# Performance work log

Measured on AMD Instinct MI355X. Metric: run time of the kernel, lower is better.

Reference implementation:

```python
import jax, jax.numpy as jnp
import numpy as np

DIM = 1024
NUM_HEADS = 16
HEAD_DIM = DIM // NUM_HEADS
SCALE = HEAD_DIM ** -0.5
HIDDEN = int(DIM * 1.0)


def setup_inputs() -> dict:
    key = jax.random.key(0)
    ks = jax.random.split(key, 11)
    s = 0.02
    return {
        "x":  jax.random.normal(ks[0], (2, 2048, DIM), jnp.float32),
        "Wq": jax.random.normal(ks[1], (DIM, DIM), jnp.float32) * s,
        "bq": jnp.zeros((DIM,), jnp.float32),
        "Wk": jax.random.normal(ks[2], (DIM, DIM), jnp.float32) * s,
        "bk": jnp.zeros((DIM,), jnp.float32),
        "Wv": jax.random.normal(ks[3], (DIM, DIM), jnp.float32) * s,
        "bv": jnp.zeros((DIM,), jnp.float32),
        "W1": jax.random.normal(ks[4], (HIDDEN, DIM), jnp.float32) * s,
        "b1": jnp.zeros((HIDDEN,), jnp.float32),
        "W2": jax.random.normal(ks[5], (DIM, HIDDEN), jnp.float32) * s,
        "b2": jnp.zeros((DIM,), jnp.float32),
    }


def _split_heads(t, B, S):
    # [B,S,C] -> [B,H,S,hd]
    return t.reshape(B, S, NUM_HEADS, HEAD_DIM).transpose(0, 2, 1, 3)


def reference(x, Wq, bq, Wk, bk, Wv, bv, W1, b1, W2, b2):
    B, S, C = x.shape
    q = _split_heads(x @ Wq.T + bq, B, S) * SCALE
    k = _split_heads(x @ Wk.T + bk, B, S)
    v = _split_heads(x @ Wv.T + bv, B, S)
    # softmax-free bilinear attention, scores in float32 (matches .float())
    attn = jnp.einsum('bhqd,bhkd->bhqk', q.astype(jnp.float32), k.astype(jnp.float32))
    out = jnp.einsum('bhqk,bhkd->bhqd', attn, v)  # [B,H,S,hd]
    out = out.transpose(0, 2, 1, 3).reshape(B, S, C)
    h = jax.nn.gelu(out @ W1.T + b1, approximate=False)
    mlp = h @ W2.T + b2
    return x + out + mlp
```

## Files before the change

### kernel.cpp

```cpp
#include <hip/hip_runtime.h>
#include <math.h>

#define DIM    1024
#define BATCH  2
#define SEQ    2048
#define NHEAD  16
#define HDIM   64
#define MROWS  (BATCH*SEQ)
#define NSPLIT 8

typedef unsigned short u16;
typedef __attribute__((ext_vector_type(8))) short  s16x8;
typedef __attribute__((ext_vector_type(4))) float  f32x4;

__device__ __forceinline__ float bf2f(u16 h) {
    unsigned u = ((unsigned)h) << 16; float f; __builtin_memcpy(&f, &u, 4); return f;
}
__device__ __forceinline__ u16 f2bf(float f) {
    unsigned u; __builtin_memcpy(&u, &f, 4);
    u += 0x7FFFu + ((u >> 16) & 1u);
    return (u16)(u >> 16);
}

__device__ __forceinline__ void glds16(const u16* g, u16* l) {
    __builtin_amdgcn_global_load_lds(
        (const __attribute__((address_space(1))) void*)g,
        (__attribute__((address_space(3))) void*)l, 16, 0, 0);
}

__global__ __launch_bounds__(256)
void pack_all(const float* __restrict__ x,
              const float* __restrict__ Wq, const float* __restrict__ Wk,
              const float* __restrict__ Wv, const float* __restrict__ W1,
              const float* __restrict__ W2,
              u16* __restrict__ xb, u16* __restrict__ Wqb, u16* __restrict__ Wkb,
              u16* __restrict__ Wvb, u16* __restrict__ W1b, u16* __restrict__ W2b)
{
    const int bid = blockIdx.x;
    const float* src; u16* dst; int i;
    if (bid < 4096) { src = x; dst = xb; i = bid * 256 + threadIdx.x; }
    else {
        const int w = (bid - 4096) >> 10;
        const int lb = (bid - 4096) & 1023;
        src = (w == 0) ? Wq : (w == 1) ? Wk : (w == 2) ? Wv : (w == 3) ? W1 : W2;
        dst = (w == 0) ? Wqb : (w == 1) ? Wkb : (w == 2) ? Wvb : (w == 3) ? W1b : W2b;
        i = lb * 256 + threadIdx.x;
    }
    float4 v = ((const float4*)src)[i];
    ushort4 o = { f2bf(v.x), f2bf(v.y), f2bf(v.z), f2bf(v.w) };
    ((ushort4*)dst)[i] = o;
}

__device__ __forceinline__ void gemm_core_pf128(const u16* __restrict__ Ab,
                                                const u16* __restrict__ Bb,
                                                u16* As, u16* Bs,
                                                int tid, f32x4 acc[4][4])
{
    const int w = tid >> 6, l = tid & 63;
    const int wm = (w >> 1) * 64, wn = (w & 1) * 64;
    const int lr = l & 15, kq = l >> 4;

    const int srow = w * 16 + (l >> 2);
    const int scol = (l & 3) * 8;
    const u16* gA = Ab + (size_t)srow * DIM + scol;
    const u16* gB = Bb + (size_t)srow * DIM + scol;
    const int sdst = w * 512;

    glds16(gA,      As + sdst);         glds16(gA + 64 * DIM,      As + 2048 + sdst);
    glds16(gB,      Bs + sdst);         glds16(gB + 64 * DIM,      Bs + 2048 + sdst);
    glds16(gA + 32, As + 4096 + sdst);  glds16(gA + 32 + 64 * DIM, As + 4096 + 2048 + sdst);
    glds16(gB + 32, Bs + 4096 + sdst);  glds16(gB + 32 + 64 * DIM, Bs + 4096 + 2048 + sdst);

    const int NIT = DIM / 32;
    int cur = 0, nxt2 = 2;
    for (int it = 0; it < NIT; ++it) {
        if (it < NIT - 1) { asm volatile("s_waitcnt vmcnt(4)" ::: "memory"); }
        else              { asm volatile("s_waitcnt vmcnt(0)" ::: "memory"); }
        __builtin_amdgcn_s_barrier();
        asm volatile("" ::: "memory");
        if (it + 2 < NIT) {
            const int k = (it + 2) * 32;
            u16* An = As + nxt2 * 4096 + sdst;
            u16* Bn = Bs + nxt2 * 4096 + sdst;
            glds16(gA + k, An);  glds16(gA + k + 64 * DIM, An + 2048);
            glds16(gB + k, Bn);  glds16(gB + k + 64 * DIM, Bn + 2048);
        }
        const u16* Ac = As + cur * 4096;
        const u16* Bc = Bs + cur * 4096;
        s16x8 af[4], bfr[4];
        #pragma unroll
        for (int i = 0; i < 4; ++i)
            af[i]  = *(const s16x8*)(Ac + (wm + i * 16 + lr) * 32 + kq * 8);
        #pragma unroll
        for (int j = 0; j < 4; ++j)
            bfr[j] = *(const s16x8*)(Bc + (wn + j * 16 + lr) * 32 + kq * 8);
        __builtin_amdgcn_s_setprio(1);
        #pragma unroll
        for (int i = 0; i < 4; ++i)
            #pragma unroll
            for (int j = 0; j < 4; ++j)
                acc[i][j] = __builtin_amdgcn_mfma_f32_16x16x32_bf16(af[i], bfr[j], acc[i][j], 0, 0, 0);
        __builtin_amdgcn_s_setprio(0);
        cur  = (cur  == 2) ? 0 : cur  + 1;
        nxt2 = (nxt2 == 2) ? 0 : nxt2 + 1;
    }
}

__global__ __launch_bounds__(256)
void qkv_gemm(const u16* __restrict__ xb,
              const u16* __restrict__ Wq, const u16* __restrict__ Wk, const u16* __restrict__ Wv,
              const float* __restrict__ bq, const float* __restrict__ bk, const float* __restrict__ bv,
              u16* __restrict__ qo, u16* __restrict__ ko, u16* __restrict__ vo)
{
    __shared__ __align__(16) u16 SH[24576];
    const int tid = threadIdx.x;
    const int m0  = blockIdx.x * 128;
    const int sel = blockIdx.y >> 3;
    const int n0  = (blockIdx.y & 7) * 128;
    const u16*   B    = (sel == 0) ? Wq : (sel == 1) ? Wk : Wv;
    const float* bias = (sel == 0) ? bq : (sel == 1) ? bk : bv;
    u16*         C    = (sel == 0) ? qo : (sel == 1) ? ko : vo;
    const float scale = (sel == 0) ? 0.125f : 1.0f;

    f32x4 acc[4][4];
    #pragma unroll
    for (int i = 0; i < 4; ++i)
        #pragma unroll
        for (int j = 0; j < 4; ++j) acc[i][j] = (f32x4){0.f, 0.f, 0.f, 0.f};

    gemm_core_pf128(xb + (size_t)m0 * DIM, B + (size_t)n0 * DIM, SH, SH + 12288, tid, acc);

    __syncthreads();
    const int w = tid >> 6, l = tid & 63;
    const int wm = (w >> 1) * 64, wn = (w & 1) * 64;
    const int er = l >> 4, ec = l & 15;
    #pragma unroll
    for (int j = 0; j < 4; ++j) {
        const int colv = wn + j * 16 + ec;
        const float bb = bias[n0 + colv];
        const int cg = colv >> 3, cl = colv & 7;
        #pragma unroll
        for (int i = 0; i < 4; ++i)
            #pragma unroll
            for (int r = 0; r < 4; ++r) {
                const int row = wm + i * 16 + er * 4 + r;
                const int g = ((row >> 2) & 3) << 1;
                SH[row * 128 + ((cg ^ g) << 3) + cl] = f2bf((acc[i][j][r] + bb) * scale);
            }
    }
    __syncthreads();
    {
        const int cg = tid & 15, rr = tid >> 4;
        #pragma unroll
        for (int pass = 0; pass < 8; ++pass) {
            const int row = rr + (pass << 4);
            const int g = ((row >> 2) & 3) << 1;
            uint4 v = *(const uint4*)(SH + row * 128 + ((cg ^ g) << 3));
            *(uint4*)(C + (size_t)(m0 + row) * DIM + n0 + (cg << 3)) = v;
        }
    }
}

__global__ __launch_bounds__(256)
void gemm_bf16(const u16* __restrict__ A, const u16* __restrict__ B,
               const float* __restrict__ bias,
               u16* __restrict__ Cb, float* __restrict__ Cf,
               const float* __restrict__ rx, const u16* __restrict__ rattn,
               int mode)
{
    __shared__ __align__(16) u16 SH[24576];
    const int tid = threadIdx.x;
    const int m0 = blockIdx.x * 128, n0 = blockIdx.y * 128;

    f32x4 acc[4][4];
    #pragma unroll
    for (int i = 0; i < 4; ++i)
        #pragma unroll
        for (int j = 0; j < 4; ++j) acc[i][j] = (f32x4){0.f, 0.f, 0.f, 0.f};

    gemm_core_pf128(A + (size_t)m0 * DIM, B + (size_t)n0 * DIM, SH, SH + 12288, tid, acc);

    const int w = tid >> 6, l = tid & 63;
    const int wm = (w >> 1) * 64, wn = (w & 1) * 64;
    const int er = l >> 4, ec = l & 15;

    if (mode == 1) {
        __syncthreads();
        #pragma unroll
        for (int j = 0; j < 4; ++j) {
            const int colv = wn + j * 16 + ec;
            const float bb = bias[n0 + colv];
            const int cg = colv >> 3, cl = colv & 7;
            #pragma unroll
            for (int i = 0; i < 4; ++i)
                #pragma unroll
                for (int r = 0; r < 4; ++r) {
                    const int row = wm + i * 16 + er * 4 + r;
                    const int g = ((row >> 2) & 3) << 1;
                    float v = acc[i][j][r] + bb;
                    v = 0.5f * v * (1.0f + erff(v * 0.70710678118654752f));
                    SH[row * 128 + ((cg ^ g) << 3) + cl] = f2bf(v);
                }
        }
        __syncthreads();
        const int cg = tid & 15, rr = tid >> 4;
        #pragma unroll
        for (int pass = 0; pass < 8; ++pass) {
            const int row = rr + (pass << 4);
            const int g = ((row >> 2) & 3) << 1;
            uint4 v = *(const uint4*)(SH + row * 128 + ((cg ^ g) << 3));
            *(uint4*)(Cb + (size_t)(m0 + row) * DIM + n0 + (cg << 3)) = v;
        }
    } else {
        float* SHF = (float*)SH;
        #pragma unroll
        for (int h = 0; h < 4; ++h) {
            __syncthreads();
            if ((wm >> 6) == (h >> 1)) {
                #pragma unroll
                for (int j = 0; j < 4; ++j) {
                    const int colv = wn + j * 16 + ec;
                    const float bb = bias[n0 + colv];
                    const int c4 = colv >> 2, c2 = colv & 3;
                    #pragma unroll
                    for (int ii = 0; ii < 2; ++ii) {
                        const int i = (h & 1) * 2 + ii;
                        #pragma unroll
                        for (int r = 0; r < 4; ++r) {
                            const int rl = ii * 16 + er * 4 + r;
                            const int g4 = ((rl >> 2) & 1) << 2;
                            SHF[rl * 128 + ((c4 ^ g4) << 2) + c2] = acc[i][j][r] + bb;
                        }
                    }
                }
            }
            __syncthreads();
            const int c4 = tid & 31, rr = tid >> 5;
            #pragma unroll
            for (int pass = 0; pass < 4; ++pass) {
                const int rl = rr + (pass << 3);
                const int g4 = ((rl >> 2) & 1) << 2;
                float4 v = *(const float4*)(SHF + rl * 128 + ((c4 ^ g4) << 2));
                const size_t idx = (size_t)(m0 + 32 * h + rl) * DIM + n0 + (c4 << 2);
                float4 rxv = *(const float4*)(rx + idx);
                ushort4 rav = *(const ushort4*)(rattn + idx);
                float4 o = { v.x + rxv.x + bf2f(rav.x),
                             v.y + rxv.y + bf2f(rav.y),
                             v.z + rxv.z + bf2f(rav.z),
                             v.w + rxv.w + bf2f(rav.w) };
                *(float4*)(Cf + idx) = o;
            }
        }
    }
}

__global__ __launch_bounds__(256)
void ktv_mfma(const u16* __restrict__ Kb, const u16* __restrict__ Vb,
              float* __restrict__ part)
{
    __shared__ u16 Kt[64 * 264];
    __shared__ u16 Vt[64 * 264];
    const int tid = threadIdx.x;
    const int bh = blockIdx.x & 31;
    const int sp = blockIdx.x >> 5;
    const int b = bh >> 4, h = bh & 15;
    const size_t base = (size_t)b * SEQ * DIM + (size_t)h * HDIM + (size_t)sp * 256 * DIM;

    const int dg = (tid & 15) * 4;
    #pragma unroll
    for (int pass = 0; pass < 16; ++pass) {
        const int s = (tid >> 4) + 16 * pass;
        ushort4 kv = *(const ushort4*)(Kb + base + (size_t)s * DIM + dg);
        ushort4 vv = *(const ushort4*)(Vb + base + (size_t)s * DIM + dg);
        Kt[(dg + 0) * 264 + s] = kv.x; Kt[(dg + 1) * 264 + s] = kv.y;
        Kt[(dg + 2) * 264 + s] = kv.z; Kt[(dg + 3) * 264 + s] = kv.w;
        Vt[(dg + 0) * 264 + s] = vv.x; Vt[(dg + 1) * 264 + s] = vv.y;
        Vt[(dg + 2) * 264 + s] = vv.z; Vt[(dg + 3) * 264 + s] = vv.w;
    }
    __syncthreads();

    const int w = tid >> 6, l = tid & 63;
    const int lr = l & 15, kq = l >> 4;
    f32x4 acc[4];
    #pragma unroll
    for (int j = 0; j < 4; ++j) acc[j] = (f32x4){0.f, 0.f, 0.f, 0.f};

    for (int k0 = 0; k0 < 256; k0 += 32) {
        s16x8 af = *(const s16x8*)(Kt + (w * 16 + lr) * 264 + k0 + kq * 8);
        #pragma unroll
        for (int j = 0; j < 4; ++j) {
            s16x8 bf = *(const s16x8*)(Vt + (j * 16 + lr) * 264 + k0 + kq * 8);
            acc[j] = __builtin_amdgcn_mfma_f32_16x16x32_bf16(af, bf, acc[j], 0, 0, 0);
        }
    }

    float* dst = part + ((size_t)sp * 32 + bh) * (HDIM * HDIM);
    const int er = l >> 4, ec = l & 15;
    #pragma unroll
    for (int j = 0; j < 4; ++j)
        #pragma unroll
        for (int r = 0; r < 4; ++r)
            dst[(w * 16 + er * 4 + r) * HDIM + j * 16 + ec] = acc[j][r];
}

__global__ __launch_bounds__(256)
void qktv_kernel(const u16* __restrict__ Qb, const float* __restrict__ part,
                 u16* __restrict__ attnb)
{
    __shared__ float KV[HDIM * HDIM];
    __shared__ u16 Qs[128 * 68];
    const int tid = threadIdx.x;
    const int h  = blockIdx.x;
    const int mt = blockIdx.y;
    const int row0 = mt * 128;
    const int b = row0 >> 11;
    const int bh = b * NHEAD + h;

    for (int i = tid; i < HDIM * HDIM; i += 256) {
        float s = 0.f;
        #pragma unroll
        for (int sp = 0; sp < NSPLIT; ++sp)
            s += part[((size_t)sp * 32 + bh) * (HDIM * HDIM) + i];
        KV[i] = s;
    }
    const int dg = (tid & 15) * 4;
    #pragma unroll
    for (int pass = 0; pass < 8; ++pass) {
        const int r = (tid >> 4) + 16 * pass;
        ushort4 q = *(const ushort4*)(Qb + (size_t)(row0 + r) * DIM + h * HDIM + dg);
        *(ushort4*)(Qs + r * 68 + dg) = q;
    }
    __syncthreads();

    const int tr = tid >> 3, tc = tid & 7;
    const int r0 = tr * 4, c0 = tc * 8;
    float acc[4][8] = {};
    for (int d = 0; d < HDIM; ++d) {
        float4 ka  = *(const float4*)&KV[d * HDIM + c0];
        float4 kb2 = *(const float4*)&KV[d * HDIM + c0 + 4];
        const float* k8a = (const float*)&ka;
        const float* k8b = (const float*)&kb2;
        float qv[4];
        #pragma unroll
        for (int i = 0; i < 4; ++i) qv[i] = bf2f(Qs[(r0 + i) * 68 + d]);
        #pragma unroll
        for (int i = 0; i < 4; ++i)
            #pragma unroll
            for (int j = 0; j < 4; ++j) {
                acc[i][j]     += qv[i] * k8a[j];
                acc[i][j + 4] += qv[i] * k8b[j];
            }
    }
    #pragma unroll
    for (int i = 0; i < 4; ++i) {
        u16* dst = attnb + (size_t)(row0 + r0 + i) * DIM + h * HDIM + c0;
        ushort4 o0 = { f2bf(acc[i][0]), f2bf(acc[i][1]), f2bf(acc[i][2]), f2bf(acc[i][3]) };
        ushort4 o1 = { f2bf(acc[i][4]), f2bf(acc[i][5]), f2bf(acc[i][6]), f2bf(acc[i][7]) };
        *(ushort4*)(dst)     = o0;
        *(ushort4*)(dst + 4) = o1;
    }
}

extern "C" void kernel_launch(void* const* d_in, const int* in_sizes, int n_in,
                              void* d_out, int out_size, void* d_ws, size_t ws_size,
                              hipStream_t stream)
{
    const float* x  = (const float*)d_in[0];
    const float* Wq = (const float*)d_in[1];
    const float* bq = (const float*)d_in[2];
    const float* Wk = (const float*)d_in[3];
    const float* bk = (const float*)d_in[4];
    const float* Wv = (const float*)d_in[5];
    const float* bv = (const float*)d_in[6];
    const float* W1 = (const float*)d_in[7];
    const float* b1 = (const float*)d_in[8];
    const float* W2 = (const float*)d_in[9];
    const float* b2 = (const float*)d_in[10];
    float* out = (float*)d_out;

    char* ws = (char*)d_ws;
    const size_t MB = 1u << 20;
    u16* xb   = (u16*)(ws);
    u16* Wqb  = (u16*)(ws +  8 * MB);
    u16* Wkb  = (u16*)(ws + 10 * MB);
    u16* Wvb  = (u16*)(ws + 12 * MB);
    u16* W1b  = (u16*)(ws + 14 * MB);
    u16* W2b  = (u16*)(ws + 16 * MB);
    u16* qb   = (u16*)(ws + 18 * MB);
    u16* kb   = (u16*)(ws + 26 * MB);
    u16* vb   = (u16*)(ws + 34 * MB);
    float* part = (float*)(ws + 42 * MB);
    u16* attnb = kb;
    u16* h1b   = vb;

    pack_all<<<4096 + 5 * 1024, 256, 0, stream>>>(x, Wq, Wk, Wv, W1, W2,
                                                  xb, Wqb, Wkb, Wvb, W1b, W2b);

    qkv_gemm<<<dim3(32, 24), 256, 0, stream>>>(xb, Wqb, Wkb, Wvb, bq, bk, bv, qb, kb, vb);

    ktv_mfma<<<NSPLIT * 32, 256, 0, stream>>>(kb, vb, part);
    qktv_kernel<<<dim3(NHEAD, MROWS / 128), 256, 0, stream>>>(qb, part, attnb);

    gemm_bf16<<<dim3(32, 8), 256, 0, stream>>>(attnb, W1b, b1, h1b, nullptr, nullptr, nullptr, 1);
    gemm_bf16<<<dim3(32, 8), 256, 0, stream>>>(h1b, W2b, b2, nullptr, out, x, attnb, 2);
}
```

Measured before the change: 195.6 us.

## Compute Q·KV with bf16 MFMA using hi/lo split of KV

Replaces the scalar FP32 FMA loop in qktv_kernel with MFMA 16x16x32 bf16 instructions. To keep accuracy, the reduced KV matrix is split into bf16 high and low residual parts stored transposed in shared memory, so each product takes two MFMAs. Q fragments are loaded straight from global memory into registers. The partial-sum reduction now uses float4 loads, and the output is staged through shared memory for coalesced 16-byte stores. Accuracy is slightly reduced because Q stays bf16 and KV is a two-term bf16 approximation.

```diff
diff --git a/kernel.cpp b/kernel.cpp
--- a/kernel.cpp
+++ b/kernel.cpp
@@ -307,8 +307,7 @@
 void qktv_kernel(const u16* __restrict__ Qb, const float* __restrict__ part,
                  u16* __restrict__ attnb)
 {
-    __shared__ float KV[HDIM * HDIM];
-    __shared__ u16 Qs[128 * 68];
+    __shared__ __align__(16) u16 SH[18432];
     const int tid = threadIdx.x;
     const int h  = blockIdx.x;
     const int mt = blockIdx.y;
@@ -316,48 +315,81 @@
     const int b = row0 >> 11;
     const int bh = b * NHEAD + h;
 
-    for (int i = tid; i < HDIM * HDIM; i += 256) {
-        float s = 0.f;
-        #pragma unroll
-        for (int sp = 0; sp < NSPLIT; ++sp)
-            s += part[((size_t)sp * 32 + bh) * (HDIM * HDIM) + i];
-        KV[i] = s;
-    }
-    const int dg = (tid & 15) * 4;
-    #pragma unroll
-    for (int pass = 0; pass < 8; ++pass) {
-        const int r = (tid >> 4) + 16 * pass;
-        ushort4 q = *(const ushort4*)(Qb + (size_t)(row0 + r) * DIM + h * HDIM + dg);
-        *(ushort4*)(Qs + r * 68 + dg) = q;
+    const int w = tid >> 6, l = tid & 63;
+    const int wm = (w >> 1) * 64, wn = (w & 1) * 32;
+    const int lr = l & 15, kq = l >> 4;
+
+    s16x8 aq[4][2];
+    #pragma unroll
+    for (int i = 0; i < 4; ++i)
+        #pragma unroll
+        for (int ks = 0; ks < 2; ++ks)
+            aq[i][ks] = *(const s16x8*)(Qb + (size_t)(row0 + wm + i * 16 + lr) * DIM
+                                        + h * HDIM + ks * 32 + kq * 8);
+
+    #pragma unroll
+    for (int p = 0; p < 4; ++p) {
+        const int c = tid + 256 * p;
+        float4 s = {0.f, 0.f, 0.f, 0.f};
+        #pragma unroll
+        for (int sp = 0; sp < NSPLIT; ++sp) {
+            float4 v = *(const float4*)(part + ((size_t)sp * 32 + bh) * 4096 + (size_t)c * 4);
+            s.x += v.x; s.y += v.y; s.z += v.z; s.w += v.w;
+        }
+        const int d1  = c >> 4;
+        const int d2b = (c & 15) * 4;
+        float sv[4] = {s.x, s.y, s.z, s.w};
+        #pragma unroll
+        for (int q = 0; q < 4; ++q) {
+            const u16 hi = f2bf(sv[q]);
+            const float rem = sv[q] - bf2f(hi);
+            SH[(d2b + q) * 72 + d1]        = hi;
+            SH[4608 + (d2b + q) * 72 + d1] = f2bf(rem);
+        }
     }
     __syncthreads();
 
-    const int tr = tid >> 3, tc = tid & 7;
-    const int r0 = tr * 4, c0 = tc * 8;
-    float acc[4][8] = {};
-    for (int d = 0; d < HDIM; ++d) {
-        float4 ka  = *(const float4*)&KV[d * HDIM + c0];
-        float4 kb2 = *(const float4*)&KV[d * HDIM + c0 + 4];
-        const float* k8a = (const float*)&ka;
-        const float* k8b = (const float*)&kb2;
-        float qv[4];
-        #pragma unroll
-        for (int i = 0; i < 4; ++i) qv[i] = bf2f(Qs[(r0 + i) * 68 + d]);
+    f32x4 acc[4][2];
+    #pragma unroll
+    for (int i = 0; i < 4; ++i)
+        #pragma unroll
+        for (int j = 0; j < 2; ++j) acc[i][j] = (f32x4){0.f, 0.f, 0.f, 0.f};
+
+    #pragma unroll
+    for (int ks = 0; ks < 2; ++ks) {
+        s16x8 bhi[2], blo[2];
+        #pragma unroll
+        for (int j = 0; j < 2; ++j) {
+            const int n = wn + j * 16 + lr;
+            bhi[j] = *(const s16x8*)(SH + n * 72 + ks * 32 + kq * 8);
+            blo[j] = *(const s16x8*)(SH + 4608 + n * 72 + ks * 32 + kq * 8);
+        }
         #pragma unroll
         for (int i = 0; i < 4; ++i)
             #pragma unroll
-            for (int j = 0; j < 4; ++j) {
-                acc[i][j]     += qv[i] * k8a[j];
-                acc[i][j + 4] += qv[i] * k8b[j];
+            for (int j = 0; j < 2; ++j) {
+                acc[i][j] = __builtin_amdgcn_mfma_f32_16x16x32_bf16(aq[i][ks], bhi[j], acc[i][j], 0, 0, 0);
+                acc[i][j] = __builtin_amdgcn_mfma_f32_16x16x32_bf16(aq[i][ks], blo[j], acc[i][j], 0, 0, 0);
             }
     }
-    #pragma unroll
-    for (int i = 0; i < 4; ++i) {
-        u16* dst = attnb + (size_t)(row0 + r0 + i) * DIM + h * HDIM + c0;
-        ushort4 o0 = { f2bf(acc[i][0]), f2bf(acc[i][1]), f2bf(acc[i][2]), f2bf(acc[i][3]) };
-        ushort4 o1 = { f2bf(acc[i][4]), f2bf(acc[i][5]), f2bf(acc[i][6]), f2bf(acc[i][7]) };
-        *(ushort4*)(dst)     = o0;
-        *(ushort4*)(dst + 4) = o1;
+
+    u16* SHB = SH + 9216;
+    const int er = l >> 4, ec = l & 15;
+    #pragma unroll
+    for (int i = 0; i < 4; ++i)
+        #pragma unroll
+        for (int j = 0; j < 2; ++j)
+            #pragma unroll
+            for (int r = 0; r < 4; ++r)
+                SHB[(wm + i * 16 + er * 4 + r) * 72 + wn + j * 16 + ec] = f2bf(acc[i][j][r]);
+    __syncthreads();
+    {
+        const int row = tid >> 1, half = tid & 1;
+        const u16* srcp = SHB + row * 72 + half * 32;
+        u16* dst = attnb + (size_t)(row0 + row) * DIM + h * HDIM + half * 32;
+        #pragma unroll
+        for (int q = 0; q < 4; ++q)
+            *(uint4*)(dst + q * 8) = *(const uint4*)(srcp + q * 8);
     }
 }
 
```

After: 198.8 us. About the same (+1.6%).

## Write K and V head-transposed from QKV GEMM and read directly in KtV

Applied to the files above, without the earlier changes.

The QKV GEMM epilogue now writes K and V in a per-head transposed [b,h,d,seq] layout by staging the tile transposed in shared memory. The K^T V kernel can then load MFMA fragments straight from global memory with contiguous 16-byte reads, dropping its shared-memory transpose, scalar LDS stores and barrier. The cost moves into the GEMM epilogue, whose scattered 2-byte LDS writes with a padded stride may bank-conflict. The q/k/v consumer signatures and host-side buffers must also match the new layout.

```diff
diff --git a/kernel.cpp b/kernel.cpp
--- a/kernel.cpp
+++ b/kernel.cpp
@@ -110,7 +110,7 @@
 void qkv_gemm(const u16* __restrict__ xb,
               const u16* __restrict__ Wq, const u16* __restrict__ Wk, const u16* __restrict__ Wv,
               const float* __restrict__ bq, const float* __restrict__ bk, const float* __restrict__ bv,
-              u16* __restrict__ qo, u16* __restrict__ ko, u16* __restrict__ vo)
+              u16* __restrict__ qo, u16* __restrict__ kT, u16* __restrict__ vT)
 {
     __shared__ __align__(16) u16 SH[24576];
     const int tid = threadIdx.x;
@@ -119,7 +119,6 @@
     const int n0  = (blockIdx.y & 7) * 128;
     const u16*   B    = (sel == 0) ? Wq : (sel == 1) ? Wk : Wv;
     const float* bias = (sel == 0) ? bq : (sel == 1) ? bk : bv;
-    u16*         C    = (sel == 0) ? qo : (sel == 1) ? ko : vo;
     const float scale = (sel == 0) ? 0.125f : 1.0f;
 
     f32x4 acc[4][4];
@@ -134,30 +133,55 @@
     const int w = tid >> 6, l = tid & 63;
     const int wm = (w >> 1) * 64, wn = (w & 1) * 64;
     const int er = l >> 4, ec = l & 15;
-    #pragma unroll
-    for (int j = 0; j < 4; ++j) {
-        const int colv = wn + j * 16 + ec;
-        const float bb = bias[n0 + colv];
-        const int cg = colv >> 3, cl = colv & 7;
-        #pragma unroll
-        for (int i = 0; i < 4; ++i)
-            #pragma unroll
-            for (int r = 0; r < 4; ++r) {
-                const int row = wm + i * 16 + er * 4 + r;
-                const int g = ((row >> 2) & 3) << 1;
-                SH[row * 128 + ((cg ^ g) << 3) + cl] = f2bf((acc[i][j][r] + bb) * scale);
-            }
-    }
-    __syncthreads();
-    {
+
+    if (sel == 0) {
+        #pragma unroll
+        for (int j = 0; j < 4; ++j) {
+            const int colv = wn + j * 16 + ec;
+            const float bb = bias[n0 + colv];
+            const int cg = colv >> 3, cl = colv & 7;
+            #pragma unroll
+            for (int i = 0; i < 4; ++i)
+                #pragma unroll
+                for (int r = 0; r < 4; ++r) {
+                    const int row = wm + i * 16 + er * 4 + r;
+                    const int g = ((row >> 2) & 3) << 1;
+                    SH[row * 128 + ((cg ^ g) << 3) + cl] = f2bf((acc[i][j][r] + bb) * scale);
+                }
+        }
+        __syncthreads();
         const int cg = tid & 15, rr = tid >> 4;
         #pragma unroll
         for (int pass = 0; pass < 8; ++pass) {
             const int row = rr + (pass << 4);
             const int g = ((row >> 2) & 3) << 1;
             uint4 v = *(const uint4*)(SH + row * 128 + ((cg ^ g) << 3));
-            *(uint4*)(C + (size_t)(m0 + row) * DIM + n0 + (cg << 3)) = v;
-        }
+            *(uint4*)(qo + (size_t)(m0 + row) * DIM + n0 + (cg << 3)) = v;
+        }
+    } else {
+        u16* dstBase = (sel == 1) ? kT : vT;
+        #pragma unroll
+        for (int j = 0; j < 4; ++j) {
+            const int colv = wn + j * 16 + ec;
+            const float bb = bias[n0 + colv];
+            #pragma unroll
+            for (int i = 0; i < 4; ++i)
+                #pragma unroll
+                for (int r = 0; r < 4; ++r) {
+                    const int row = wm + i * 16 + er * 4 + r;
+                    SH[colv * 136 + row] = f2bf(acc[i][j][r] + bb);
+                }
+        }
+        __syncthreads();
+        const int n = tid >> 1, half = tid & 1;
+        const int colg = n0 + n;
+        const int hh = colg >> 6, d = colg & 63;
+        const int b = m0 >> 11, s0 = m0 & 2047;
+        u16* dstp = dstBase + (((size_t)(b * NHEAD + hh) * HDIM + d) * SEQ) + s0 + half * 64;
+        const u16* srcp = SH + n * 136 + half * 64;
+        #pragma unroll
+        for (int q = 0; q < 8; ++q)
+            *(uint4*)(dstp + q * 8) = *(const uint4*)(srcp + q * 8);
     }
 }
 
@@ -255,41 +279,30 @@
 }
 
 __global__ __launch_bounds__(256)
-void ktv_mfma(const u16* __restrict__ Kb, const u16* __restrict__ Vb,
+void ktv_mfma(const u16* __restrict__ kT, const u16* __restrict__ vT,
               float* __restrict__ part)
 {
-    __shared__ u16 Kt[64 * 264];
-    __shared__ u16 Vt[64 * 264];
     const int tid = threadIdx.x;
     const int bh = blockIdx.x & 31;
     const int sp = blockIdx.x >> 5;
-    const int b = bh >> 4, h = bh & 15;
-    const size_t base = (size_t)b * SEQ * DIM + (size_t)h * HDIM + (size_t)sp * 256 * DIM;
-
-    const int dg = (tid & 15) * 4;
-    #pragma unroll
-    for (int pass = 0; pass < 16; ++pass) {
-        const int s = (tid >> 4) + 16 * pass;
-        ushort4 kv = *(const ushort4*)(Kb + base + (size_t)s * DIM + dg);
-        ushort4 vv = *(const ushort4*)(Vb + base + (size_t)s * DIM + dg);
-        Kt[(dg + 0) * 264 + s] = kv.x; Kt[(dg + 1) * 264 + s] = kv.y;
-        Kt[(dg + 2) * 264 + s] = kv.z; Kt[(dg + 3) * 264 + s] = kv.w;
-        Vt[(dg + 0) * 264 + s] = vv.x; Vt[(dg + 1) * 264 + s] = vv.y;
-        Vt[(dg + 2) * 264 + s] = vv.z; Vt[(dg + 3) * 264 + s] = vv.w;
-    }
-    __syncthreads();
-
     const int w = tid >> 6, l = tid & 63;
     const int lr = l & 15, kq = l >> 4;
+
+    const u16* Ap = kT + (size_t)bh * (HDIM * SEQ) + (size_t)(w * 16 + lr) * SEQ
+                       + sp * 256 + kq * 8;
+    const u16* Bp = vT + (size_t)bh * (HDIM * SEQ) + (size_t)lr * SEQ
+                       + sp * 256 + kq * 8;
+
     f32x4 acc[4];
     #pragma unroll
     for (int j = 0; j < 4; ++j) acc[j] = (f32x4){0.f, 0.f, 0.f, 0.f};
 
+    #pragma unroll
     for (int k0 = 0; k0 < 256; k0 += 32) {
-        s16x8 af = *(const s16x8*)(Kt + (w * 16 + lr) * 264 + k0 + kq * 8);
+        s16x8 af = *(const s16x8*)(Ap + k0);
         #pragma unroll
         for (int j = 0; j < 4; ++j) {
-            s16x8 bf = *(const s16x8*)(Vt + (j * 16 + lr) * 264 + k0 + kq * 8);
+            s16x8 bf = *(const s16x8*)(Bp + (size_t)j * 16 * SEQ + k0);
             acc[j] = __builtin_amdgcn_mfma_f32_16x16x32_bf16(af, bf, acc[j], 0, 0, 0);
         }
     }
```

Result: slower. 204.0 us (+4.3%).
